# Kernel tuning notes

Hardware: AMD Instinct MI355X
Metric: run time of the kernel (lower is better)

## Reference

```python
import jax, jax.numpy as jnp
import numpy as np
from jax import lax

NUM_ITER = 40
NO_PAD = (0, 0)
PAD1 = (1, 1)


def _min_pool(x, window, padding):
    # torch's -max_pool(-x) with implicit -inf padding == min-pool with +inf padding
    return lax.reduce_window(x, jnp.array(jnp.inf, x.dtype), lax.min,
                             window, (1, 1, 1, 1), padding)


def _max_pool(x, window, padding):
    return lax.reduce_window(x, jnp.array(-jnp.inf, x.dtype), lax.max,
                             window, (1, 1, 1, 1), padding)


def soft_erode(img):
    # min over 3x1 and 1x3 windows, then elementwise min (4D / 2D image path)
    p1 = _min_pool(img, (1, 1, 3, 1), (NO_PAD, NO_PAD, PAD1, NO_PAD))
    p2 = _min_pool(img, (1, 1, 1, 3), (NO_PAD, NO_PAD, NO_PAD, PAD1))
    return jnp.minimum(p1, p2)


def soft_dilate(img):
    return _max_pool(img, (1, 1, 3, 3), (NO_PAD, NO_PAD, PAD1, PAD1))


def soft_open(img):
    return soft_dilate(soft_erode(img))


def soft_skel(img):
    skel = jax.nn.relu(img - soft_open(img))

    def step(carry, _):
        img, skel = carry
        img = soft_erode(img)
        delta = jax.nn.relu(img - soft_open(img))
        skel = skel + jax.nn.relu(delta - skel * delta)
        return (img, skel), None

    (_, skel), _ = lax.scan(step, (img, skel), None, length=NUM_ITER)
    return skel


def setup_inputs() -> dict:
    key = jax.random.key(0)
    img = jax.random.uniform(key, (4, 1, 1024, 1024), dtype=jnp.float32)  # values in [0,1]
    return {"img": img}


def reference(img):
    return soft_skel(img)
```

## Files before the change

kernel.cpp:

```cpp
#include <hip/hip_runtime.h>
#include <math.h>

#define WID 1024
#define HEI 1024
#define OUTC 48
#define HALOC 8
#define BH 16
#define CB 22
#define RB 64

__device__ __forceinline__ float lane_up1(float v) {
    return __int_as_float(__builtin_amdgcn_update_dpp(
        __float_as_int(v), __float_as_int(v), 0x138, 0xF, 0xF, false));
}
__device__ __forceinline__ float lane_dn1(float v) {
    return __int_as_float(__builtin_amdgcn_update_dpp(
        __float_as_int(v), __float_as_int(v), 0x130, 0xF, 0xF, false));
}
__device__ __forceinline__ float fmin3(float a, float b, float c) {
    float d; asm("v_min3_f32 %0, %1, %2, %3" : "=v"(d) : "v"(a), "v"(b), "v"(c));
    return d;
}
__device__ __forceinline__ float fmax3(float a, float b, float c) {
    float d; asm("v_max3_f32 %0, %1, %2, %3" : "=v"(d) : "v"(a), "v"(b), "v"(c));
    return d;
}

template<int K, bool FIRST, bool WIMG, bool EDGE>
__device__ __forceinline__ void body4(const float* __restrict__ imgp,
                                      float* __restrict__ outi,
                                      float* __restrict__ outs,
                                      int r0, int x, int xc, bool colIn, bool outLane)
{
    constexpr int FILL  = ((K & 3) == 3) ? (K + 6) : (K + 8);
    constexpr int NSTEP = (BH + 20) / 4;
    const float INF = INFINITY;

    float c[K+1], d[K+1], sk[16];
    #pragma unroll
    for (int j = 0; j <= K; ++j) { c[j] = INF; d[j] = INF; }
    #pragma unroll
    for (int t = 0; t < 16; ++t) sk[t] = 0.f;

    float vI[4], vS[4] = {0.f, 0.f, 0.f, 0.f};

    #pragma unroll
    for (int q = 0; q < 4; ++q) {
        const int rr = 1 - FILL + q;
        if (EDGE) {
            int row = r0 + rr;
            bool rin = (unsigned)row < (unsigned)HEI;
            int rowc = row < 0 ? 0 : (row > HEI-1 ? HEI-1 : row);
            float v = imgp[(size_t)rowc * WID + xc];
            vI[q] = (rin && colIn) ? v : INF;
        } else {
            vI[q] = imgp[(size_t)(r0 + rr) * WID + x];
        }
    }

    #pragma unroll
    for (int n = 1; n <= NSTEP; ++n) {
        float bp[6] = { c[0], d[0], vI[0], vI[1], vI[2], vI[3] };
        c[0] = bp[4]; d[0] = bp[5];

        #pragma unroll
        for (int q = 0; q < 4; ++q) {
            const int rrE = 4*n - FILL - 5 + q;
            if (rrE >= 0 && rrE < BH) sk[rrE & 15] = FIRST ? 0.f : vS[q];
        }

        if (n < NSTEP) {
            #pragma unroll
            for (int q = 0; q < 4; ++q) {
                const int rr = 4*(n+1) - FILL - 3 + q;
                if (EDGE) {
                    int row = r0 + rr;
                    bool rin = (unsigned)row < (unsigned)HEI;
                    int rowc = row < 0 ? 0 : (row > HEI-1 ? HEI-1 : row);
                    float v = imgp[(size_t)rowc * WID + xc];
                    vI[q] = (rin && colIn) ? v : INF;
                } else {
                    vI[q] = imgp[(size_t)(r0 + rr) * WID + x];
                }
            }
            if (!FIRST) {
                #pragma unroll
                for (int q = 0; q < 4; ++q) {
                    const int rrL = 4*(n+1) - FILL - 5 + q;
                    if (rrL >= 0 && rrL < BH)
                        vS[q] = EDGE ? outs[(size_t)(r0 + rrL) * WID + xc]
                                     : outs[(size_t)(r0 + rrL) * WID + x];
                }
            }
        }

        float eK[6];

        #pragma unroll
        for (int j = 1; j <= K; ++j) {
            float o[4];
            #pragma unroll
            for (int q = 0; q < 4; ++q) {
                float up = bp[q], ce = bp[q+1], dn = bp[q+2];
                float lf = lane_up1(ce), rt = lane_dn1(ce);
                float pre = fmin3(up, ce, lf);
                float nj  = fmin3(pre, rt, dn);
                if (EDGE) {
                    const int rr = 4*n - FILL - 3 - j + q;
                    bool rin = (unsigned)(r0 + rr) < (unsigned)HEI;
                    nj = (rin && colIn) ? nj : INF;
                }
                o[q] = nj;
            }
            float bc[6] = { c[j], d[j], o[0], o[1], o[2], o[3] };
            c[j] = bc[4]; d[j] = bc[5];

            {
                const int t = j - 1;
                #pragma unroll
                for (int q = 0; q < 4; ++q) {
                    const int rr = 4*n - FILL - 5 - t + q;
                    float a0 = bc[q], a1 = bc[q+1], a2 = bc[q+2];
                    if (EDGE) {
                        bool i0 = (unsigned)(r0 + rr - 1) < (unsigned)HEI;
                        bool i1 = (unsigned)(r0 + rr    ) < (unsigned)HEI;
                        bool i2 = (unsigned)(r0 + rr + 1) < (unsigned)HEI;
                        a0 = i0 ? a0 : -INF;
                        a1 = i1 ? a1 : -INF;
                        a2 = i2 ? a2 : -INF;
                    }
                    float vm = fmax3(a0, a1, a2);
                    if (EDGE) vm = colIn ? vm : -INF;
                    float hl = lane_up1(vm), hr = lane_dn1(vm);
                    float dd = fmax3(hl, hr, vm);
                    float delta = fmaxf(bp[q] - dd, 0.f);
                    float sv = sk[rr & 15];
                    sk[rr & 15] = sv + fmaf(-sv, delta, delta);
                }
            }
            #pragma unroll
            for (int p = 0; p < 6; ++p) bp[p] = bc[p];
            if (j == K) {
                #pragma unroll
                for (int p = 0; p < 6; ++p) eK[p] = bc[p];
            }
        }

        #pragma unroll
        for (int q = 0; q < 4; ++q) {
            const int rr = 4*n - 24 + q;
            if (rr >= 0 && rr < BH) {
                if (outLane) outs[(size_t)(r0 + rr) * WID + x] = sk[rr & 15];
                if (WIMG) { if (outLane) outi[(size_t)(r0 + rr) * WID + x] = eK[1 + q]; }
            }
        }
    }
}

template<int K, bool FIRST, bool WIMG>
__global__ __launch_bounds__(256, 3)
void pass_kernel(const float* __restrict__ img_in, float* __restrict__ img_out,
                 float* __restrict__ skel)
{
    const int lane = threadIdx.x & 63;
    const int warp = threadIdx.x >> 6;
    const int bid   = blockIdx.x;
    const int rbg   = bid & 7;
    const int rest  = bid >> 3;
    const int sub   = rest & 1;
    const int rest2 = rest >> 1;
    const int cb    = rest2 % CB;
    const int b     = rest2 / CB;
    const int rb    = rbg*8 + sub*4 + warp;

    const int outc = (cb == CB-1) ? (WID - (CB-1)*OUTC) : OUTC;
    const int x0   = cb*OUTC - HALOC;
    const int r0   = rb*BH;
    const int x    = x0 + lane;
    const int xc   = x < 0 ? 0 : (x > WID-1 ? WID-1 : x);
    const bool colIn   = ((unsigned)x < (unsigned)WID);
    const bool outLane = (lane >= HALOC) && (lane < HALOC + outc);
    const size_t base = (size_t)b*HEI*WID;

    const float* imgp = img_in + base;
    float* outi = WIMG ? (img_out + base) : nullptr;
    float* outs = skel + base;

    const bool edge = (cb == 0) || (cb == CB-1) || (rb == 0) || (rb == RB-1);
    if (edge)
        body4<K, FIRST, WIMG, true >(imgp, outi, outs, r0, x, xc, colIn, outLane);
    else
        body4<K, FIRST, WIMG, false>(imgp, outi, outs, r0, x, xc, colIn, outLane);
}

extern "C" void kernel_launch(void* const* d_in, const int* in_sizes, int n_in,
                              void* d_out, int out_size, void* d_ws, size_t ws_size,
                              hipStream_t stream)
{
    const float* img = (const float*)d_in[0];
    float* skel = (float*)d_out;
    const int total = in_sizes[0];
    const int B = total / (HEI*WID);

    float* bufA = (float*)d_ws;
    float* bufB = bufA + (size_t)total;

    const int blocks = 8 * 2 * CB * B;

    pass_kernel<7,true, true ><<<blocks,256,0,stream>>>(img,  bufA, skel);
    pass_kernel<7,false,true ><<<blocks,256,0,stream>>>(bufA, bufB, skel);
    pass_kernel<7,false,true ><<<blocks,256,0,stream>>>(bufB, bufA, skel);
    pass_kernel<7,false,true ><<<blocks,256,0,stream>>>(bufA, bufB, skel);
    pass_kernel<7,false,true ><<<blocks,256,0,stream>>>(bufB, bufA, skel);
    pass_kernel<6,false,false><<<blocks,256,0,stream>>>(bufA, nullptr, skel);
}
```

Before: 165.3 us.

## Process two columns per lane with float2 to shrink column halo overhead

Each lane now handles two adjacent columns through float2 loads and stores, so a 64-lane wave covers 128 columns with an 8-column halo on each side, producing 112 output columns instead of 48. Horizontal neighbours within a lane pair are taken directly, and cross-lane DPP shifts are applied only to the edge element. This is meant to cut redundant halo recomputation and halve the number of column blocks while vectorizing memory access. In exchange, register use per thread roughly doubles, which may hurt occupancy under the 3-wave launch bound.

```diff
diff --git a/kernel.cpp b/kernel.cpp
--- a/kernel.cpp
+++ b/kernel.cpp
@@ -3,10 +3,9 @@
 
 #define WID 1024
 #define HEI 1024
-#define OUTC 48
-#define HALOC 8
+#define OUTC 112
 #define BH 16
-#define CB 22
+#define CB 10
 #define RB 64
 
 __device__ __forceinline__ float lane_up1(float v) {
@@ -36,13 +35,15 @@
     constexpr int NSTEP = (BH + 20) / 4;
     const float INF = INFINITY;
 
-    float c[K+1], d[K+1], sk[16];
-    #pragma unroll
-    for (int j = 0; j <= K; ++j) { c[j] = INF; d[j] = INF; }
-    #pragma unroll
-    for (int t = 0; t < 16; ++t) sk[t] = 0.f;
-
-    float vI[4], vS[4] = {0.f, 0.f, 0.f, 0.f};
+    float2 c[K+1], d[K+1], sk[16];
+    #pragma unroll
+    for (int j = 0; j <= K; ++j) { c[j] = make_float2(INF, INF); d[j] = make_float2(INF, INF); }
+    #pragma unroll
+    for (int t = 0; t < 16; ++t) sk[t] = make_float2(0.f, 0.f);
+
+    float2 vI[4], vS[4];
+    #pragma unroll
+    for (int q = 0; q < 4; ++q) vS[q] = make_float2(0.f, 0.f);
 
     #pragma unroll
     for (int q = 0; q < 4; ++q) {
@@ -51,22 +52,23 @@
             int row = r0 + rr;
             bool rin = (unsigned)row < (unsigned)HEI;
             int rowc = row < 0 ? 0 : (row > HEI-1 ? HEI-1 : row);
-            float v = imgp[(size_t)rowc * WID + xc];
-            vI[q] = (rin && colIn) ? v : INF;
+            float2 v = *(const float2*)&imgp[(size_t)rowc * WID + xc];
+            bool ok = rin && colIn;
+            vI[q] = make_float2(ok ? v.x : INF, ok ? v.y : INF);
         } else {
-            vI[q] = imgp[(size_t)(r0 + rr) * WID + x];
+            vI[q] = *(const float2*)&imgp[(size_t)(r0 + rr) * WID + x];
         }
     }
 
     #pragma unroll
     for (int n = 1; n <= NSTEP; ++n) {
-        float bp[6] = { c[0], d[0], vI[0], vI[1], vI[2], vI[3] };
+        float2 bp[6] = { c[0], d[0], vI[0], vI[1], vI[2], vI[3] };
         c[0] = bp[4]; d[0] = bp[5];
 
         #pragma unroll
         for (int q = 0; q < 4; ++q) {
             const int rrE = 4*n - FILL - 5 + q;
-            if (rrE >= 0 && rrE < BH) sk[rrE & 15] = FIRST ? 0.f : vS[q];
+            if (rrE >= 0 && rrE < BH) sk[rrE & 15] = FIRST ? make_float2(0.f, 0.f) : vS[q];
         }
 
         if (n < NSTEP) {
@@ -77,10 +79,11 @@
                     int row = r0 + rr;
                     bool rin = (unsigned)row < (unsigned)HEI;
                     int rowc = row < 0 ? 0 : (row > HEI-1 ? HEI-1 : row);
-                    float v = imgp[(size_t)rowc * WID + xc];
-                    vI[q] = (rin && colIn) ? v : INF;
+                    float2 v = *(const float2*)&imgp[(size_t)rowc * WID + xc];
+                    bool ok = rin && colIn;
+                    vI[q] = make_float2(ok ? v.x : INF, ok ? v.y : INF);
                 } else {
-                    vI[q] = imgp[(size_t)(r0 + rr) * WID + x];
+                    vI[q] = *(const float2*)&imgp[(size_t)(r0 + rr) * WID + x];
                 }
             }
             if (!FIRST) {
@@ -88,31 +91,35 @@
                 for (int q = 0; q < 4; ++q) {
                     const int rrL = 4*(n+1) - FILL - 5 + q;
                     if (rrL >= 0 && rrL < BH)
-                        vS[q] = EDGE ? outs[(size_t)(r0 + rrL) * WID + xc]
-                                     : outs[(size_t)(r0 + rrL) * WID + x];
-                }
-            }
-        }
-
-        float eK[6];
+                        vS[q] = EDGE ? *(const float2*)&outs[(size_t)(r0 + rrL) * WID + xc]
+                                     : *(const float2*)&outs[(size_t)(r0 + rrL) * WID + x];
+                }
+            }
+        }
+
+        float2 eK[6];
 
         #pragma unroll
         for (int j = 1; j <= K; ++j) {
-            float o[4];
+            float2 o[4];
             #pragma unroll
             for (int q = 0; q < 4; ++q) {
-                float up = bp[q], ce = bp[q+1], dn = bp[q+2];
-                float lf = lane_up1(ce), rt = lane_dn1(ce);
-                float pre = fmin3(up, ce, lf);
-                float nj  = fmin3(pre, rt, dn);
+                float2 up = bp[q], ce = bp[q+1], dn = bp[q+2];
+                float vx = fmin3(up.x, ce.x, dn.x);
+                float vy = fmin3(up.y, ce.y, dn.y);
+                float lf = lane_up1(ce.y);
+                float rt = lane_dn1(ce.x);
+                float njx = fmin3(vx, lf, ce.y);
+                float njy = fmin3(vy, ce.x, rt);
                 if (EDGE) {
                     const int rr = 4*n - FILL - 3 - j + q;
-                    bool rin = (unsigned)(r0 + rr) < (unsigned)HEI;
-                    nj = (rin && colIn) ? nj : INF;
-                }
-                o[q] = nj;
-            }
-            float bc[6] = { c[j], d[j], o[0], o[1], o[2], o[3] };
+                    bool ok = ((unsigned)(r0 + rr) < (unsigned)HEI) && colIn;
+                    njx = ok ? njx : INF;
+                    njy = ok ? njy : INF;
+                }
+                o[q] = make_float2(njx, njy);
+            }
+            float2 bc[6] = { c[j], d[j], o[0], o[1], o[2], o[3] };
             c[j] = bc[4]; d[j] = bc[5];
 
             {
@@ -120,22 +127,30 @@
                 #pragma unroll
                 for (int q = 0; q < 4; ++q) {
                     const int rr = 4*n - FILL - 5 - t + q;
-                    float a0 = bc[q], a1 = bc[q+1], a2 = bc[q+2];
+                    float2 a0 = bc[q], a1 = bc[q+1], a2 = bc[q+2];
                     if (EDGE) {
                         bool i0 = (unsigned)(r0 + rr - 1) < (unsigned)HEI;
                         bool i1 = (unsigned)(r0 + rr    ) < (unsigned)HEI;
                         bool i2 = (unsigned)(r0 + rr + 1) < (unsigned)HEI;
-                        a0 = i0 ? a0 : -INF;
-                        a1 = i1 ? a1 : -INF;
-                        a2 = i2 ? a2 : -INF;
+                        a0 = make_float2(i0 ? a0.x : -INF, i0 ? a0.y : -INF);
+                        a1 = make_float2(i1 ? a1.x : -INF, i1 ? a1.y : -INF);
+                        a2 = make_float2(i2 ? a2.x : -INF, i2 ? a2.y : -INF);
                     }
-                    float vm = fmax3(a0, a1, a2);
-                    if (EDGE) vm = colIn ? vm : -INF;
-                    float hl = lane_up1(vm), hr = lane_dn1(vm);
-                    float dd = fmax3(hl, hr, vm);
-                    float delta = fmaxf(bp[q] - dd, 0.f);
-                    float sv = sk[rr & 15];
-                    sk[rr & 15] = sv + fmaf(-sv, delta, delta);
+                    float vmx = fmax3(a0.x, a1.x, a2.x);
+                    float vmy = fmax3(a0.y, a1.y, a2.y);
+                    if (EDGE) {
+                        vmx = colIn ? vmx : -INF;
+                        vmy = colIn ? vmy : -INF;
+                    }
+                    float hl = lane_up1(vmy);
+                    float hr = lane_dn1(vmx);
+                    float ddx = fmax3(vmx, hl, vmy);
+                    float ddy = fmax3(vmy, vmx, hr);
+                    float dex = fmaxf(bp[q].x - ddx, 0.f);
+                    float dey = fmaxf(bp[q].y - ddy, 0.f);
+                    float2 sv = sk[rr & 15];
+                    sk[rr & 15] = make_float2(sv.x + fmaf(-sv.x, dex, dex),
+                                              sv.y + fmaf(-sv.y, dey, dey));
                 }
             }
             #pragma unroll
@@ -150,8 +165,10 @@
         for (int q = 0; q < 4; ++q) {
             const int rr = 4*n - 24 + q;
             if (rr >= 0 && rr < BH) {
-                if (outLane) outs[(size_t)(r0 + rr) * WID + x] = sk[rr & 15];
-                if (WIMG) { if (outLane) outi[(size_t)(r0 + rr) * WID + x] = eK[1 + q]; }
+                if (outLane) {
+                    *(float2*)&outs[(size_t)(r0 + rr) * WID + x] = sk[rr & 15];
+                    if (WIMG) *(float2*)&outi[(size_t)(r0 + rr) * WID + x] = eK[1 + q];
+                }
             }
         }
     }
@@ -174,12 +191,12 @@
     const int rb    = rbg*8 + sub*4 + warp;
 
     const int outc = (cb == CB-1) ? (WID - (CB-1)*OUTC) : OUTC;
-    const int x0   = cb*OUTC - HALOC;
+    const int x0   = cb*OUTC - 8;
+    const int x    = x0 + 2*lane;
+    const int xc   = x < 0 ? 0 : (x > WID-2 ? WID-2 : x);
+    const bool colIn   = ((unsigned)x < (unsigned)WID);
+    const bool outLane = (lane >= 4) && (lane < 4 + outc/2);
     const int r0   = rb*BH;
-    const int x    = x0 + lane;
-    const int xc   = x < 0 ? 0 : (x > WID-1 ? WID-1 : x);
-    const bool colIn   = ((unsigned)x < (unsigned)WID);
-    const bool outLane = (lane >= HALOC) && (lane < HALOC + outc);
     const size_t base = (size_t)b*HEI*WID;
 
     const float* imgp = img_in + base;
```

Result: slower. 410.4 us (+148.3%).
